# Optimization experiments

Hardware: AMD Instinct MI355X
Metric: run time of the kernel (lower is better)

Reference implementation:

```python
import jax, jax.numpy as jnp
import numpy as np


def _hfreq_mask(c, scale):
    # zeros over the centered (shifted) low-frequency band, ones elsewhere
    m = np.ones((c,), dtype=np.complex64)
    m[c // 2 - c // scale: c // 2 + c // scale] = 0
    return jnp.asarray(m).reshape(1, 1, 1, c)


def setup_inputs() -> dict:
    key = jax.random.key(0)
    x = jax.random.normal(key, (32, 38, 38, 728), dtype=jnp.float32)
    return {"x": x, "scale": 4}


def reference(x, scale):
    c = x.shape[-1]
    norm = jnp.asarray(np.sqrt(c), dtype=jnp.complex64)
    X = jnp.fft.fft(x.astype(jnp.complex64), axis=-1) / norm
    X = jnp.fft.fftshift(X, axes=-1)
    X = X * _hfreq_mask(c, scale)
    X = jnp.fft.ifftshift(X, axes=-1)
    y = jnp.fft.ifft(X, axis=-1) * norm
    y = jnp.real(y).astype(jnp.float32)
    return jax.nn.relu(y)
```

## Files before the change

### kernel.cpp

```cpp
#include <hip/hip_runtime.h>
#include <hip/hip_bf16.h>

#define CC 728
#define PP 364
#define KP 384
#define M_ROWS 46208
#define KT 12
#define NWG 2166

typedef __attribute__((ext_vector_type(8))) short bf16x8;
typedef __attribute__((ext_vector_type(8))) unsigned short ushort8;
typedef __attribute__((ext_vector_type(4))) float f32x4;

__device__ __forceinline__ unsigned short f2bf(float f) {
    unsigned int u = __float_as_uint(f);
    unsigned int r = u + 0x7fffu + ((u >> 16) & 1u);
    return (unsigned short)(r >> 16);
}

__device__ __forceinline__ void gload_lds16(const void* g, void* l) {
    __builtin_amdgcn_global_load_lds(
        (const __attribute__((address_space(1))) void*)g,
        (__attribute__((address_space(3))) void*)l,
        16, 0, 0);
}

__global__ void build_bt(unsigned short* __restrict__ bt1,
                         unsigned short* __restrict__ bt2) {
    int idx = blockIdx.x * blockDim.x + threadIdx.x;
    if (idx >= 2 * KP * KP) return;
    int mat = idx / (KP * KP);
    int rem = idx % (KP * KP);
    int n = rem / KP, k = rem % KP;
    float v = 0.f;
    if (n < PP && k < PP) {
        int m = n - k - (mat == 0 ? 1 : 0);
        if (m < 0) m += PP;
        int d = 2 * m + 1;
        float t = (float)(3.14159265358979323846 * (double)d / (double)CC);
        float s = ((d >> 1) & 1) ? 1.f : -1.f;
        v = s * cosf(t) / ((float)CC * sinf(t));
    }
    (mat == 0 ? bt1 : bt2)[n * KP + k] = f2bf(v);
}

__global__ __launch_bounds__(256) void gemm_relu(
        const float* __restrict__ x,
        const unsigned short* __restrict__ bt1,
        const unsigned short* __restrict__ bt2,
        float* __restrict__ out) {
    __shared__ unsigned short ldsE[2][64 * 32];
    __shared__ unsigned short ldsO[2][64 * 32];
    __shared__ unsigned short ldsB1[2][128 * 32];
    __shared__ unsigned short ldsB2[2][128 * 32];

    const int tid  = threadIdx.x;
    const int lane = tid & 63;
    const int wid  = tid >> 6;
    const int wr   = wid >> 1, wc = wid & 1;
    const int l15  = lane & 15, lhi = lane >> 4;

    const int NX = 8;
    int orig = blockIdx.x;
    int q = NWG / NX, r = NWG % NX;
    int xcd = orig % NX, local = orig / NX;
    int wgid = (xcd < r ? xcd * (q + 1) : r * (q + 1) + (xcd - r) * q) + local;
    const int bm  = (wgid / 3) * 64;
    const int bnp = (wgid % 3) * 128;

    f32x4 acc_e[2][4], acc_o[2][4];
#pragma unroll
    for (int i = 0; i < 2; ++i)
#pragma unroll
        for (int j = 0; j < 4; ++j)
#pragma unroll
            for (int rr = 0; rr < 4; ++rr) { acc_e[i][j][rr] = 0.f; acc_o[i][j][rr] = 0.f; }

    const int brow = tid >> 2;
    const int bc   = tid & 3;
    const int arow = tid >> 2;
    const int acx  = tid & 3;

    auto stageB = [&](int buf, int k0) {
#pragma unroll
        for (int i = 0; i < 2; ++i) {
            int rr   = i * 64 + brow;
            int gsrc = (bc - (rr >> 1)) & 3;
            size_t so = (size_t)(bnp + rr) * KP + k0 + gsrc * 8;
            gload_lds16(bt1 + so, &ldsB1[buf][(i * 256 + tid) * 8]);
            gload_lds16(bt2 + so, &ldsB2[buf][(i * 256 + tid) * 8]);
        }
    };
    auto loadA = [&](int k0, float4* va) {
        int cb0 = 2 * k0 + acx * 16;
        const float* src = x + (size_t)(bm + arow) * CC + cb0;
#pragma unroll
        for (int i = 0; i < 4; ++i)
            va[i] = (cb0 + 4 * i < CC) ? ((const float4*)src)[i]
                                       : make_float4(0.f, 0.f, 0.f, 0.f);
    };
    auto writeA = [&](int buf, const float4* va) {
        ushort8 oe, oo;
#pragma unroll
        for (int p = 0; p < 4; ++p) {
            float4 f = va[p];
            oe[2 * p]     = f2bf(f.x); oo[2 * p]     = f2bf(f.y);
            oe[2 * p + 1] = f2bf(f.z); oo[2 * p + 1] = f2bf(f.w);
        }
        int sc = (acx + (arow >> 1)) & 3;
        *(ushort8*)&ldsE[buf][arow * 32 + sc * 8] = oe;
        *(ushort8*)&ldsO[buf][arow * 32 + sc * 8] = oo;
    };

    {
        float4 va[4];
        stageB(0, 0);
        loadA(0, va);
        writeA(0, va);
    }
    __syncthreads();

    int cur = 0;
    for (int kt = 0; kt < KT; ++kt) {
        const int nxt = cur ^ 1;
        const bool more = (kt + 1 < KT);

        float4 va2[4];
        if (more) {
            stageB(nxt, (kt + 1) * 32);
            loadA((kt + 1) * 32, va2);
        }

        bf16x8 aE[2], aO[2], b1[4], b2[4];
#pragma unroll
        for (int mi = 0; mi < 2; ++mi) {
            int row = wr * 32 + mi * 16 + l15;
            int c   = (lhi + (row >> 1)) & 3;
            aE[mi] = *(const bf16x8*)&ldsE[cur][row * 32 + c * 8];
            aO[mi] = *(const bf16x8*)&ldsO[cur][row * 32 + c * 8];
        }
#pragma unroll
        for (int nj = 0; nj < 4; ++nj) {
            int row = wc * 64 + nj * 16 + l15;
            int c   = (lhi + (row >> 1)) & 3;
            b1[nj] = *(const bf16x8*)&ldsB1[cur][row * 32 + c * 8];
            b2[nj] = *(const bf16x8*)&ldsB2[cur][row * 32 + c * 8];
        }
#pragma unroll
        for (int mi = 0; mi < 2; ++mi)
#pragma unroll
            for (int nj = 0; nj < 4; ++nj) {
                acc_e[mi][nj] = __builtin_amdgcn_mfma_f32_16x16x32_bf16(
                    aO[mi], b1[nj], acc_e[mi][nj], 0, 0, 0);
                acc_o[mi][nj] = __builtin_amdgcn_mfma_f32_16x16x32_bf16(
                    aE[mi], b2[nj], acc_o[mi][nj], 0, 0, 0);
            }

        if (more) writeA(nxt, va2);

        __syncthreads();
        cur = nxt;
    }

#pragma unroll
    for (int mi = 0; mi < 2; ++mi) {
#pragma unroll
        for (int nj = 0; nj < 4; ++nj) {
            int colp = bnp + wc * 64 + nj * 16 + l15;
            if (colp < PP) {
#pragma unroll
                for (int rr = 0; rr < 4; ++rr) {
                    int rowg = bm + wr * 32 + mi * 16 + lhi * 4 + rr;
                    size_t base = (size_t)rowg * CC + 2 * colp;
                    float2 xv = *(const float2*)&x[base];
                    float2 o;
                    float ye = 0.5f * xv.x + acc_e[mi][nj][rr];
                    float yo = 0.5f * xv.y + acc_o[mi][nj][rr];
                    o.x = ye > 0.f ? ye : 0.f;
                    o.y = yo > 0.f ? yo : 0.f;
                    *(float2*)&out[base] = o;
                }
            }
        }
    }
}

extern "C" void kernel_launch(void* const* d_in, const int* in_sizes, int n_in,
                              void* d_out, int out_size, void* d_ws, size_t ws_size,
                              hipStream_t stream) {
    const float* x = (const float*)d_in[0];
    float* out = (float*)d_out;

    unsigned short* bt1 = (unsigned short*)d_ws;
    unsigned short* bt2 = bt1 + KP * KP;

    build_bt<<<(2 * KP * KP + 255) / 256, 256, 0, stream>>>(bt1, bt2);
    gemm_relu<<<NWG, 256, 0, stream>>>(x, bt1, bt2, out);
}
```

Baseline: 112.6 us.

## Triple-buffer LDS with two-deep prefetch and a single barrier per K step

Moves the GEMM main loop from double to triple LDS buffering. A and B tiles are now prefetched two K-steps ahead, with manual vmcnt/lgkmcnt waits and one s_barrier per iteration in place of the trailing __syncthreads. It also raises wave priority around the MFMA block and fully unrolls the K loop. The goal is to hide global-load latency behind compute. The cost is more LDS per workgroup, which may lower occupancy, and hand-tuned waitcnt values that must match the exact count of issued loads. The out-of-range tail steps keep the same number of loads in flight by issuing redundant loads of tile 10.

```diff
diff --git a/kernel.cpp b/kernel.cpp
--- a/kernel.cpp
+++ b/kernel.cpp
@@ -49,10 +49,10 @@
         const unsigned short* __restrict__ bt1,
         const unsigned short* __restrict__ bt2,
         float* __restrict__ out) {
-    __shared__ unsigned short ldsE[2][64 * 32];
-    __shared__ unsigned short ldsO[2][64 * 32];
-    __shared__ unsigned short ldsB1[2][128 * 32];
-    __shared__ unsigned short ldsB2[2][128 * 32];
+    __shared__ unsigned short ldsE[3][64 * 32];
+    __shared__ unsigned short ldsO[3][64 * 32];
+    __shared__ unsigned short ldsB1[3][128 * 32];
+    __shared__ unsigned short ldsB2[3][128 * 32];
 
     const int tid  = threadIdx.x;
     const int lane = tid & 63;
@@ -81,7 +81,8 @@
     const int arow = tid >> 2;
     const int acx  = tid & 3;
 
-    auto stageB = [&](int buf, int k0) {
+    auto stageB = [&](int buf, int kt) {
+        int k0 = kt * 32;
 #pragma unroll
         for (int i = 0; i < 2; ++i) {
             int rr   = i * 64 + brow;
@@ -91,8 +92,8 @@
             gload_lds16(bt2 + so, &ldsB2[buf][(i * 256 + tid) * 8]);
         }
     };
-    auto loadA = [&](int k0, float4* va) {
-        int cb0 = 2 * k0 + acx * 16;
+    auto loadA = [&](int kt, float4* va) {
+        int cb0 = kt * 64 + acx * 16;
         const float* src = x + (size_t)(bm + arow) * CC + cb0;
 #pragma unroll
         for (int i = 0; i < 4; ++i)
@@ -112,24 +113,24 @@
         *(ushort8*)&ldsO[buf][arow * 32 + sc * 8] = oo;
     };
 
-    {
-        float4 va[4];
-        stageB(0, 0);
-        loadA(0, va);
-        writeA(0, va);
-    }
-    __syncthreads();
+    float4 va[2][4];
+    loadA(0, va[0]); stageB(0, 0);
+    loadA(1, va[1]); stageB(1, 1);
 
-    int cur = 0;
+#pragma unroll
     for (int kt = 0; kt < KT; ++kt) {
-        const int nxt = cur ^ 1;
-        const bool more = (kt + 1 < KT);
+        const int cur = kt % 3;
+        const int nx2 = (kt + 2) % 3;
 
-        float4 va2[4];
-        if (more) {
-            stageB(nxt, (kt + 1) * 32);
-            loadA((kt + 1) * 32, va2);
-        }
+        asm volatile("s_waitcnt vmcnt(8)" ::: "memory");
+        writeA(cur, va[kt & 1]);
+        asm volatile("s_waitcnt lgkmcnt(0)" ::: "memory");
+        __builtin_amdgcn_s_barrier();
+        __builtin_amdgcn_sched_barrier(0);
+
+        const int kpre = (kt + 2 < KT) ? (kt + 2) : 10;
+        loadA(kpre, va[kt & 1]);
+        stageB(nx2, kpre);
 
         bf16x8 aE[2], aO[2], b1[4], b2[4];
 #pragma unroll
@@ -146,6 +147,7 @@
             b1[nj] = *(const bf16x8*)&ldsB1[cur][row * 32 + c * 8];
             b2[nj] = *(const bf16x8*)&ldsB2[cur][row * 32 + c * 8];
         }
+        __builtin_amdgcn_s_setprio(1);
 #pragma unroll
         for (int mi = 0; mi < 2; ++mi)
 #pragma unroll
@@ -155,11 +157,7 @@
                 acc_o[mi][nj] = __builtin_amdgcn_mfma_f32_16x16x32_bf16(
                     aE[mi], b2[nj], acc_o[mi][nj], 0, 0, 0);
             }
-
-        if (more) writeA(nxt, va2);
-
-        __syncthreads();
-        cur = nxt;
+        __builtin_amdgcn_s_setprio(0);
     }
 
 #pragma unroll
```

Result: faster. 107.8 us (-4.3%).
